# Kernel tuning notes

Hardware: AMD Instinct MI355X
Metric: run time of the kernel (lower is better)

Reference implementation:

```python
import jax, jax.numpy as jnp
import numpy as np

BATCH = 4096  # number of rows in the sparse input matrix (static for segment_sum)


def setup_inputs() -> dict:
    key = jax.random.key(0)
    k1, k2, k3, k4 = jax.random.split(key, 4)
    nnz = 262144
    in_features, out_features = 32000, 256
    row_idx = jnp.sort(jax.random.randint(k1, (nnz,), 0, BATCH, dtype=jnp.int32))
    col_idx = jax.random.randint(k2, (nnz,), 0, in_features, dtype=jnp.int32)
    vals = jax.random.uniform(k3, (nnz,), dtype=jnp.float32)
    weight = jax.random.normal(k4, (in_features, out_features), dtype=jnp.float32) / np.sqrt(out_features)
    bias = jnp.zeros((out_features,), dtype=jnp.float32)
    return {"row_idx": row_idx, "col_idx": col_idx, "vals": vals,
            "weight": weight, "bias": bias}


def reference(row_idx, col_idx, vals, weight, bias):
    # out = sparse_input @ weight + bias
    # sparse_input is COO: (row_idx, col_idx, vals), shape [BATCH, in_features]
    # gather weight rows for each nonzero, scale by value, sum per output row
    contrib = vals[:, None] * weight[col_idx]          # [nnz, out_features]
    out = jax.ops.segment_sum(contrib, row_idx, num_segments=BATCH)  # [BATCH, out]
    return out + bias
```

## Files before the change

kernel.cpp:

```cpp
#include <hip/hip_runtime.h>


constexpr int BATCH = 4096;

__global__ __launch_bounds__(256) void prep_quant(
    const float* __restrict__ weight,
    unsigned*    __restrict__ wq,
    float*       __restrict__ scale,
    const int*   __restrict__ row_idx, int nnz,
    int*         __restrict__ ptr,
    int in_f, int conv_blocks)
{
    if ((int)blockIdx.x < conv_blocks) {
        const int wave = threadIdx.x >> 6;
        const int lane = threadIdx.x & 63;
        const int r    = blockIdx.x * 4 + wave;
        if (r < in_f) {
            const float4 f = reinterpret_cast<const float4*>(weight)[r * 64 + lane];
            float m = fmaxf(fmaxf(fabsf(f.x), fabsf(f.y)),
                            fmaxf(fabsf(f.z), fabsf(f.w)));
            #pragma unroll
            for (int o = 32; o; o >>= 1) m = fmaxf(m, __shfl_xor(m, o));
            const float inv = (m > 0.f) ? 127.0f / m : 0.0f;
            const int q0 = (int)rintf(f.x * inv);
            const int q1 = (int)rintf(f.y * inv);
            const int q2 = (int)rintf(f.z * inv);
            const int q3 = (int)rintf(f.w * inv);
            const unsigned p = ( (unsigned)q0        & 0xFFu)
                             | (((unsigned)q1 & 0xFFu) <<  8)
                             | (((unsigned)q2 & 0xFFu) << 16)
                             | (((unsigned)q3 & 0xFFu) << 24);
            wq[(size_t)r * 64 + lane] = p;
            if (lane == 0) scale[r] = (m > 0.f) ? m / 127.0f : 0.0f;
        }
    } else {
        const int i = ((int)blockIdx.x - conv_blocks) * 256 + threadIdx.x;
        if (i >= nnz) return;
        const int r  = row_idx[i];
        const int rn = (i + 1 < nnz) ? row_idx[i + 1] : BATCH;
        for (int rr = r + 1; rr <= rn; ++rr) ptr[rr] = i + 1;
        if (i == 0)
            for (int rr = 0; rr <= r; ++rr) ptr[rr] = 0;
    }
}

__global__ __launch_bounds__(256) void prep_vals(
    const int*   __restrict__ col_idx,
    const float* __restrict__ vals,
    const float* __restrict__ scale,
    float*       __restrict__ vsc, int nnz)
{
    const int i = blockIdx.x * 256 + threadIdx.x;
    if (i < nnz) vsc[i] = vals[i] * scale[col_idx[i]];
}

__device__ inline void fma8(float v, uint2 w, float* acc) {
    const unsigned ux = w.x, uy = w.y;
    acc[0] = fmaf(v, (float)((int)(ux << 24) >> 24), acc[0]);
    acc[1] = fmaf(v, (float)((int)(ux << 16) >> 24), acc[1]);
    acc[2] = fmaf(v, (float)((int)(ux <<  8) >> 24), acc[2]);
    acc[3] = fmaf(v, (float)((int) ux        >> 24), acc[3]);
    acc[4] = fmaf(v, (float)((int)(uy << 24) >> 24), acc[4]);
    acc[5] = fmaf(v, (float)((int)(uy << 16) >> 24), acc[5]);
    acc[6] = fmaf(v, (float)((int)(uy <<  8) >> 24), acc[6]);
    acc[7] = fmaf(v, (float)((int) uy        >> 24), acc[7]);
}

__global__ __launch_bounds__(256, 8) void spmm_i8(
    const int*      __restrict__ col_idx,
    const float*    __restrict__ vsc,
    const unsigned* __restrict__ wq,
    const float*    __restrict__ bias,
    const int*      __restrict__ ptr,
    float*          __restrict__ out)
{
    __shared__ float part[4][32][8];

    const int wave = threadIdx.x >> 6;
    const int lane = threadIdx.x & 63;
    const int r    = blockIdx.x * 2 + (wave >> 1);
    const int half = wave & 1;
    const int h32  = lane >> 5;
    const int c32  = lane & 31;

    const int start = ptr[r];
    const int end   = ptr[r + 1];
    const int chunk = (end - start + 1) >> 1;

    int k  = start + half * chunk;
    const int ke = min(k + chunk, end);

    const uint2* __restrict__ W2 = reinterpret_cast<const uint2*>(wq);

    float acc[8] = {0.f, 0.f, 0.f, 0.f, 0.f, 0.f, 0.f, 0.f};

    while (k + 16 <= ke) {
        int cs[8]; float vs[8]; uint2 ws[8];
        #pragma unroll
        for (int t = 0; t < 8; ++t) {
            const int kk = k + 2 * t + h32;
            cs[t] = col_idx[kk];
            vs[t] = vsc[kk];
        }
        #pragma unroll
        for (int t = 0; t < 8; ++t)
            ws[t] = W2[(size_t)cs[t] * 32 + c32];
        #pragma unroll
        for (int t = 0; t < 8; ++t)
            fma8(vs[t], ws[t], acc);
        k += 16;
    }
    while (k < ke) {
        const int  kk    = k + h32;
        const bool valid = kk < ke;
        const int   c = col_idx[valid ? kk : start];
        const float v = valid ? vsc[kk] : 0.0f;
        const uint2 w = W2[(size_t)c * 32 + c32];
        fma8(v, w, acc);
        k += 2;
    }

    #pragma unroll
    for (int d = 0; d < 8; ++d) acc[d] += __shfl_xor(acc[d], 32);

    if (lane < 32) {
        #pragma unroll
        for (int d = 0; d < 8; ++d) part[wave][lane][d] = acc[d];
    }
    __syncthreads();

    if (threadIdx.x < 128) {
        const int rl = threadIdx.x >> 6;
        const int ln = threadIdx.x & 63;
        const int ci = ln >> 1;
        const int co = (ln & 1) * 4;
        const float4 b = reinterpret_cast<const float4*>(bias)[ln];
        float4 o;
        o.x = part[2*rl][ci][co+0] + part[2*rl+1][ci][co+0] + b.x;
        o.y = part[2*rl][ci][co+1] + part[2*rl+1][ci][co+1] + b.y;
        o.z = part[2*rl][ci][co+2] + part[2*rl+1][ci][co+2] + b.z;
        o.w = part[2*rl][ci][co+3] + part[2*rl+1][ci][co+3] + b.w;
        reinterpret_cast<float4*>(out)[(size_t)(blockIdx.x * 2 + rl) * 64 + ln] = o;
    }
}

extern "C" void kernel_launch(void* const* d_in, const int* in_sizes, int n_in,
                              void* d_out, int out_size, void* d_ws, size_t ws_size,
                              hipStream_t stream)
{
    const int*   row_idx = (const int*)  d_in[0];
    const int*   col_idx = (const int*)  d_in[1];
    const float* vals    = (const float*)d_in[2];
    const float* weight  = (const float*)d_in[3];
    const float* bias    = (const float*)d_in[4];
    float*       out     = (float*)      d_out;
    const int    nnz     = in_sizes[0];
    const int    in_f    = in_sizes[3] / 256;

    unsigned* wq      = (unsigned*)d_ws;
    float*    scale   = (float*)((char*)d_ws + (12u << 20));
    int*      row_ptr = (int*)  ((char*)d_ws + (13u << 20));
    float*    vsc     = (float*)((char*)d_ws + (14u << 20));

    const int conv_blocks = (in_f + 3) / 4;
    const int rptr_blocks = (nnz + 255) / 256;

    hipLaunchKernelGGL(prep_quant, dim3(conv_blocks + rptr_blocks), dim3(256), 0, stream,
                       weight, wq, scale, row_idx, nnz, row_ptr, in_f, conv_blocks);
    hipLaunchKernelGGL(prep_vals, dim3((nnz + 255) / 256), dim3(256), 0, stream,
                       col_idx, vals, scale, vsc, nnz);
    hipLaunchKernelGGL(spmm_i8, dim3(BATCH / 2), dim3(256), 0, stream,
                       col_idx, vsc, wq, bias, row_ptr, out);
}
```

Measured before the change: 104.0 us.

## Slice quantized weights by output columns and schedule row groups per XCC via atomics

The int8 weight is re-laid out into eight column slices of 32 outputs each, so each slice (about 1 MB) can stay resident in one XCC's L2. Waves read their XCC id and start on that slice, then pull groups of 8 rows from a per-slice atomic counter, moving to the other slices once their own is drained. The separate vals*scale prep kernel is dropped and the scaling is folded into the gather loop. In exchange, col_idx and vals are re-read once per slice (eight times in total), there are atomic contention and per-row shuffle reductions, and only 4 output columns are accumulated per lane.

After: 239.1 us. +129.9%, slower.

```diff
diff --git a/kernel.cpp b/kernel.cpp
--- a/kernel.cpp
+++ b/kernel.cpp
@@ -2,6 +2,8 @@
 
 
 constexpr int BATCH = 4096;
+constexpr int ROWS_PER_GRP = 8;
+constexpr int NGRP = BATCH / ROWS_PER_GRP;
 
 __global__ __launch_bounds__(256) void prep_quant(
     const float* __restrict__ weight,
@@ -9,6 +11,7 @@
     float*       __restrict__ scale,
     const int*   __restrict__ row_idx, int nnz,
     int*         __restrict__ ptr,
+    int*         __restrict__ cnt,
     int in_f, int conv_blocks)
 {
     if ((int)blockIdx.x < conv_blocks) {
@@ -30,11 +33,15 @@
                              | (((unsigned)q1 & 0xFFu) <<  8)
                              | (((unsigned)q2 & 0xFFu) << 16)
                              | (((unsigned)q3 & 0xFFu) << 24);
-            wq[(size_t)r * 64 + lane] = p;
+            const int s    = lane >> 3;
+            const int cpos = lane & 7;
+            wq[((size_t)s * in_f + r) * 8 + cpos] = p;
             if (lane == 0) scale[r] = (m > 0.f) ? m / 127.0f : 0.0f;
         }
     } else {
-        const int i = ((int)blockIdx.x - conv_blocks) * 256 + threadIdx.x;
+        const int b = (int)blockIdx.x - conv_blocks;
+        if (b == 0) cnt[threadIdx.x] = 0;
+        const int i = b * 256 + threadIdx.x;
         if (i >= nnz) return;
         const int r  = row_idx[i];
         const int rn = (i + 1 < nnz) ? row_idx[i + 1] : BATCH;
@@ -44,103 +51,71 @@
     }
 }
 
-__global__ __launch_bounds__(256) void prep_vals(
-    const int*   __restrict__ col_idx,
-    const float* __restrict__ vals,
-    const float* __restrict__ scale,
-    float*       __restrict__ vsc, int nnz)
-{
-    const int i = blockIdx.x * 256 + threadIdx.x;
-    if (i < nnz) vsc[i] = vals[i] * scale[col_idx[i]];
-}
-
-__device__ inline void fma8(float v, uint2 w, float* acc) {
-    const unsigned ux = w.x, uy = w.y;
-    acc[0] = fmaf(v, (float)((int)(ux << 24) >> 24), acc[0]);
-    acc[1] = fmaf(v, (float)((int)(ux << 16) >> 24), acc[1]);
-    acc[2] = fmaf(v, (float)((int)(ux <<  8) >> 24), acc[2]);
-    acc[3] = fmaf(v, (float)((int) ux        >> 24), acc[3]);
-    acc[4] = fmaf(v, (float)((int)(uy << 24) >> 24), acc[4]);
-    acc[5] = fmaf(v, (float)((int)(uy << 16) >> 24), acc[5]);
-    acc[6] = fmaf(v, (float)((int)(uy <<  8) >> 24), acc[6]);
-    acc[7] = fmaf(v, (float)((int) uy        >> 24), acc[7]);
-}
-
-__global__ __launch_bounds__(256, 8) void spmm_i8(
+__global__ __launch_bounds__(256, 8) void spmm_slice_q(
     const int*      __restrict__ col_idx,
-    const float*    __restrict__ vsc,
+    const float*    __restrict__ vals,
     const unsigned* __restrict__ wq,
+    const float*    __restrict__ scale,
     const float*    __restrict__ bias,
     const int*      __restrict__ ptr,
-    float*          __restrict__ out)
+    int*            __restrict__ cnt,
+    float*          __restrict__ out,
+    int in_f)
 {
-    __shared__ float part[4][32][8];
+    const int lane = threadIdx.x & 63;
+    const int j    = lane >> 3;
+    const int cpos = lane & 7;
 
-    const int wave = threadIdx.x >> 6;
-    const int lane = threadIdx.x & 63;
-    const int r    = blockIdx.x * 2 + (wave >> 1);
-    const int half = wave & 1;
-    const int h32  = lane >> 5;
-    const int c32  = lane & 31;
+    unsigned xcc;
+    asm volatile("s_getreg_b32 %0, hwreg(HW_REG_XCC_ID)" : "=s"(xcc));
 
-    const int start = ptr[r];
-    const int end   = ptr[r + 1];
-    const int chunk = (end - start + 1) >> 1;
+    for (int si = 0; si < 8; ++si) {
+        const int s = (int)((xcc + si) & 7u);
+        const unsigned* __restrict__ Ws = wq + (size_t)s * in_f * 8;
+        const float4 b = reinterpret_cast<const float4*>(bias)[s * 8 + cpos];
 
-    int k  = start + half * chunk;
-    const int ke = min(k + chunk, end);
+        for (;;) {
+            int grp = 0;
+            if (lane == 0) grp = atomicAdd(&cnt[s * 32], 1);
+            grp = __shfl(grp, 0);
+            if (grp >= NGRP) break;
 
-    const uint2* __restrict__ W2 = reinterpret_cast<const uint2*>(wq);
+            const int r0 = grp * ROWS_PER_GRP;
+            #pragma unroll 1
+            for (int rr = 0; rr < ROWS_PER_GRP; ++rr) {
+                const int r     = r0 + rr;
+                const int start = ptr[r];
+                const int end   = ptr[r + 1];
 
-    float acc[8] = {0.f, 0.f, 0.f, 0.f, 0.f, 0.f, 0.f, 0.f};
+                float a0 = 0.f, a1 = 0.f, a2 = 0.f, a3 = 0.f;
 
-    while (k + 16 <= ke) {
-        int cs[8]; float vs[8]; uint2 ws[8];
-        #pragma unroll
-        for (int t = 0; t < 8; ++t) {
-            const int kk = k + 2 * t + h32;
-            cs[t] = col_idx[kk];
-            vs[t] = vsc[kk];
+                for (int k = start; k < end; k += 8) {
+                    const int  kk    = k + j;
+                    const bool valid = kk < end;
+                    const int   c = col_idx[valid ? kk : start];
+                    const float v = valid ? vals[kk] * scale[c] : 0.0f;
+                    const unsigned w = Ws[(size_t)c * 8 + cpos];
+                    a0 = fmaf(v, (float)((int)(w << 24) >> 24), a0);
+                    a1 = fmaf(v, (float)((int)(w << 16) >> 24), a1);
+                    a2 = fmaf(v, (float)((int)(w <<  8) >> 24), a2);
+                    a3 = fmaf(v, (float)((int) w        >> 24), a3);
+                }
+
+                a0 += __shfl_xor(a0, 8);  a1 += __shfl_xor(a1, 8);
+                a2 += __shfl_xor(a2, 8);  a3 += __shfl_xor(a3, 8);
+                a0 += __shfl_xor(a0, 16); a1 += __shfl_xor(a1, 16);
+                a2 += __shfl_xor(a2, 16); a3 += __shfl_xor(a3, 16);
+                a0 += __shfl_xor(a0, 32); a1 += __shfl_xor(a1, 32);
+                a2 += __shfl_xor(a2, 32); a3 += __shfl_xor(a3, 32);
+
+                if (lane < 8) {
+                    float4 o;
+                    o.x = a0 + b.x; o.y = a1 + b.y;
+                    o.z = a2 + b.z; o.w = a3 + b.w;
+                    reinterpret_cast<float4*>(out)[(size_t)r * 64 + s * 8 + lane] = o;
+                }
+            }
         }
-        #pragma unroll
-        for (int t = 0; t < 8; ++t)
-            ws[t] = W2[(size_t)cs[t] * 32 + c32];
-        #pragma unroll
-        for (int t = 0; t < 8; ++t)
-            fma8(vs[t], ws[t], acc);
-        k += 16;
-    }
-    while (k < ke) {
-        const int  kk    = k + h32;
-        const bool valid = kk < ke;
-        const int   c = col_idx[valid ? kk : start];
-        const float v = valid ? vsc[kk] : 0.0f;
-        const uint2 w = W2[(size_t)c * 32 + c32];
-        fma8(v, w, acc);
-        k += 2;
-    }
-
-    #pragma unroll
-    for (int d = 0; d < 8; ++d) acc[d] += __shfl_xor(acc[d], 32);
-
-    if (lane < 32) {
-        #pragma unroll
-        for (int d = 0; d < 8; ++d) part[wave][lane][d] = acc[d];
-    }
-    __syncthreads();
-
-    if (threadIdx.x < 128) {
-        const int rl = threadIdx.x >> 6;
-        const int ln = threadIdx.x & 63;
-        const int ci = ln >> 1;
-        const int co = (ln & 1) * 4;
-        const float4 b = reinterpret_cast<const float4*>(bias)[ln];
-        float4 o;
-        o.x = part[2*rl][ci][co+0] + part[2*rl+1][ci][co+0] + b.x;
-        o.y = part[2*rl][ci][co+1] + part[2*rl+1][ci][co+1] + b.y;
-        o.z = part[2*rl][ci][co+2] + part[2*rl+1][ci][co+2] + b.z;
-        o.w = part[2*rl][ci][co+3] + part[2*rl+1][ci][co+3] + b.w;
-        reinterpret_cast<float4*>(out)[(size_t)(blockIdx.x * 2 + rl) * 64 + ln] = o;
     }
 }
 
@@ -160,15 +135,13 @@
     unsigned* wq      = (unsigned*)d_ws;
     float*    scale   = (float*)((char*)d_ws + (12u << 20));
     int*      row_ptr = (int*)  ((char*)d_ws + (13u << 20));
-    float*    vsc     = (float*)((char*)d_ws + (14u << 20));
+    int*      cnt     = (int*)  ((char*)d_ws + (14u << 20));
 
     const int conv_blocks = (in_f + 3) / 4;
     const int rptr_blocks = (nnz + 255) / 256;
 
     hipLaunchKernelGGL(prep_quant, dim3(conv_blocks + rptr_blocks), dim3(256), 0, stream,
-                       weight, wq, scale, row_idx, nnz, row_ptr, in_f, conv_blocks);
-    hipLaunchKernelGGL(prep_vals, dim3((nnz + 255) / 256), dim3(256), 0, stream,
-                       col_idx, vals, scale, vsc, nnz);
-    hipLaunchKernelGGL(spmm_i8, dim3(BATCH / 2), dim3(256), 0, stream,
-                       col_idx, vsc, wq, bias, row_ptr, out);
+                       weight, wq, scale, row_idx, nnz, row_ptr, cnt, in_f, conv_blocks);
+    hipLaunchKernelGGL(spmm_slice_q, dim3(2048), dim3(256), 0, stream,
+                       col_idx, vals, wq, scale, bias, row_ptr, cnt, out, in_f);
 }
```

## Map one wave per row with 16-byte int8 weight loads and shuffle-only reduction

Applied to the files above, without the earlier changes.

The SpMM kernel now gives each output row to a single wave instead of splitting it across two waves. Each lane loads a uint4 holding 16 int8 weights, so 16 lanes cover a 256-wide weight row and 4 nonzeros are processed per step. The cross-wave reduction through shared memory and the __syncthreads are replaced by two xor-shuffles, and bias is added in registers before 16 lanes write the output. The aim is fewer load instructions per byte and no block-level sync. In exchange each lane holds 16 accumulators, occupancy is capped at 4 blocks per CU, and long rows get less parallelism.

After: 101.7 us. 1.02x faster.

```diff
diff --git a/kernel.cpp b/kernel.cpp
--- a/kernel.cpp
+++ b/kernel.cpp
@@ -54,93 +54,94 @@
     if (i < nnz) vsc[i] = vals[i] * scale[col_idx[i]];
 }
 
-__device__ inline void fma8(float v, uint2 w, float* acc) {
-    const unsigned ux = w.x, uy = w.y;
-    acc[0] = fmaf(v, (float)((int)(ux << 24) >> 24), acc[0]);
-    acc[1] = fmaf(v, (float)((int)(ux << 16) >> 24), acc[1]);
-    acc[2] = fmaf(v, (float)((int)(ux <<  8) >> 24), acc[2]);
-    acc[3] = fmaf(v, (float)((int) ux        >> 24), acc[3]);
-    acc[4] = fmaf(v, (float)((int)(uy << 24) >> 24), acc[4]);
-    acc[5] = fmaf(v, (float)((int)(uy << 16) >> 24), acc[5]);
-    acc[6] = fmaf(v, (float)((int)(uy <<  8) >> 24), acc[6]);
-    acc[7] = fmaf(v, (float)((int) uy        >> 24), acc[7]);
+__device__ inline void fma16(float v, uint4 w, float* acc) {
+    const unsigned u0 = w.x, u1 = w.y, u2 = w.z, u3 = w.w;
+    acc[ 0] = fmaf(v, (float)((int)(u0 << 24) >> 24), acc[ 0]);
+    acc[ 1] = fmaf(v, (float)((int)(u0 << 16) >> 24), acc[ 1]);
+    acc[ 2] = fmaf(v, (float)((int)(u0 <<  8) >> 24), acc[ 2]);
+    acc[ 3] = fmaf(v, (float)((int) u0        >> 24), acc[ 3]);
+    acc[ 4] = fmaf(v, (float)((int)(u1 << 24) >> 24), acc[ 4]);
+    acc[ 5] = fmaf(v, (float)((int)(u1 << 16) >> 24), acc[ 5]);
+    acc[ 6] = fmaf(v, (float)((int)(u1 <<  8) >> 24), acc[ 6]);
+    acc[ 7] = fmaf(v, (float)((int) u1        >> 24), acc[ 7]);
+    acc[ 8] = fmaf(v, (float)((int)(u2 << 24) >> 24), acc[ 8]);
+    acc[ 9] = fmaf(v, (float)((int)(u2 << 16) >> 24), acc[ 9]);
+    acc[10] = fmaf(v, (float)((int)(u2 <<  8) >> 24), acc[10]);
+    acc[11] = fmaf(v, (float)((int) u2        >> 24), acc[11]);
+    acc[12] = fmaf(v, (float)((int)(u3 << 24) >> 24), acc[12]);
+    acc[13] = fmaf(v, (float)((int)(u3 << 16) >> 24), acc[13]);
+    acc[14] = fmaf(v, (float)((int)(u3 <<  8) >> 24), acc[14]);
+    acc[15] = fmaf(v, (float)((int) u3        >> 24), acc[15]);
 }
 
-__global__ __launch_bounds__(256, 8) void spmm_i8(
-    const int*      __restrict__ col_idx,
-    const float*    __restrict__ vsc,
-    const unsigned* __restrict__ wq,
-    const float*    __restrict__ bias,
-    const int*      __restrict__ ptr,
-    float*          __restrict__ out)
+__global__ __launch_bounds__(256, 4) void spmm_i8w(
+    const int*   __restrict__ col_idx,
+    const float* __restrict__ vsc,
+    const uint4* __restrict__ W4,
+    const float* __restrict__ bias,
+    const int*   __restrict__ ptr,
+    float*       __restrict__ out)
 {
-    __shared__ float part[4][32][8];
-
     const int wave = threadIdx.x >> 6;
     const int lane = threadIdx.x & 63;
-    const int r    = blockIdx.x * 2 + (wave >> 1);
-    const int half = wave & 1;
-    const int h32  = lane >> 5;
-    const int c32  = lane & 31;
+    const int g    = lane >> 4;
+    const int cpos = lane & 15;
 
+    const int r     = blockIdx.x * 4 + wave;
     const int start = ptr[r];
     const int end   = ptr[r + 1];
-    const int chunk = (end - start + 1) >> 1;
 
-    int k  = start + half * chunk;
-    const int ke = min(k + chunk, end);
+    float acc[16];
+    #pragma unroll
+    for (int i = 0; i < 16; ++i) acc[i] = 0.f;
 
-    const uint2* __restrict__ W2 = reinterpret_cast<const uint2*>(wq);
-
-    float acc[8] = {0.f, 0.f, 0.f, 0.f, 0.f, 0.f, 0.f, 0.f};
-
-    while (k + 16 <= ke) {
-        int cs[8]; float vs[8]; uint2 ws[8];
+    int k = start;
+    while (k + 32 <= end) {
+        int cs[8]; float vs[8];
         #pragma unroll
         for (int t = 0; t < 8; ++t) {
-            const int kk = k + 2 * t + h32;
+            const int kk = k + 4 * t + g;
             cs[t] = col_idx[kk];
             vs[t] = vsc[kk];
         }
+        uint4 ws[8];
         #pragma unroll
         for (int t = 0; t < 8; ++t)
-            ws[t] = W2[(size_t)cs[t] * 32 + c32];
+            ws[t] = W4[(size_t)cs[t] * 16 + cpos];
         #pragma unroll
         for (int t = 0; t < 8; ++t)
-            fma8(vs[t], ws[t], acc);
-        k += 16;
+            fma16(vs[t], ws[t], acc);
+        k += 32;
     }
-    while (k < ke) {
-        const int  kk    = k + h32;
-        const bool valid = kk < ke;
+    while (k < end) {
+        const int  kk    = k + g;
+        const bool valid = kk < end;
         const int   c = col_idx[valid ? kk : start];
         const float v = valid ? vsc[kk] : 0.0f;
-        const uint2 w = W2[(size_t)c * 32 + c32];
-        fma8(v, w, acc);
-        k += 2;
+        const uint4 w = W4[(size_t)c * 16 + cpos];
+        fma16(v, w, acc);
+        k += 4;
     }
 
     #pragma unroll
-    for (int d = 0; d < 8; ++d) acc[d] += __shfl_xor(acc[d], 32);
+    for (int i = 0; i < 16; ++i) {
+        acc[i] += __shfl_xor(acc[i], 16);
+        acc[i] += __shfl_xor(acc[i], 32);
+    }
 
-    if (lane < 32) {
+    if (lane < 16) {
+        const float4* __restrict__ B4 = reinterpret_cast<const float4*>(bias);
+        float4* __restrict__ O4 = reinterpret_cast<float4*>(out);
         #pragma unroll
-        for (int d = 0; d < 8; ++d) part[wave][lane][d] = acc[d];
-    }
-    __syncthreads();
-
-    if (threadIdx.x < 128) {
-        const int rl = threadIdx.x >> 6;
-        const int ln = threadIdx.x & 63;
-        const int ci = ln >> 1;
-        const int co = (ln & 1) * 4;
-        const float4 b = reinterpret_cast<const float4*>(bias)[ln];
-        float4 o;
-        o.x = part[2*rl][ci][co+0] + part[2*rl+1][ci][co+0] + b.x;
-        o.y = part[2*rl][ci][co+1] + part[2*rl+1][ci][co+1] + b.y;
-        o.z = part[2*rl][ci][co+2] + part[2*rl+1][ci][co+2] + b.z;
-        o.w = part[2*rl][ci][co+3] + part[2*rl+1][ci][co+3] + b.w;
-        reinterpret_cast<float4*>(out)[(size_t)(blockIdx.x * 2 + rl) * 64 + ln] = o;
+        for (int i = 0; i < 4; ++i) {
+            const float4 b = B4[cpos * 4 + i];
+            float4 o;
+            o.x = acc[4 * i + 0] + b.x;
+            o.y = acc[4 * i + 1] + b.y;
+            o.z = acc[4 * i + 2] + b.z;
+            o.w = acc[4 * i + 3] + b.w;
+            O4[(size_t)r * 64 + cpos * 4 + i] = o;
+        }
     }
 }
 
@@ -169,6 +170,6 @@
                        weight, wq, scale, row_idx, nnz, row_ptr, in_f, conv_blocks);
     hipLaunchKernelGGL(prep_vals, dim3((nnz + 255) / 256), dim3(256), 0, stream,
                        col_idx, vals, scale, vsc, nnz);
-    hipLaunchKernelGGL(spmm_i8, dim3(BATCH / 2), dim3(256), 0, stream,
-                       col_idx, vsc, wq, bias, row_ptr, out);
+    hipLaunchKernelGGL(spmm_i8w, dim3(BATCH / 4), dim3(256), 0, stream,
+                       col_idx, vsc, (const uint4*)wq, bias, row_ptr, out);
 }
```
